# Kernel tuning notes

Measured on AMD Instinct MI355X. Metric: run time of the kernel, lower is better.

Reference implementation:

```python
import jax, jax.numpy as jnp
import numpy as np

B, S, D, H = 2, 2048, 1024, 16
HD = D // H


def setup_inputs() -> dict:
    key = jax.random.key(0)
    ks = jax.random.split(key, 7)
    scale = 1.0 / np.sqrt(D)
    x = jax.random.normal(ks[0], (B, S, D), dtype=jnp.float32)
    att_mask = jax.random.randint(ks[1], (B, S, S), 0, 2, dtype=jnp.int32)
    Wq = jax.random.normal(ks[2], (D, D), dtype=jnp.float32) * scale
    Wk = jax.random.normal(ks[3], (D, D), dtype=jnp.float32) * scale
    Wv = jax.random.normal(ks[4], (D, D), dtype=jnp.float32) * scale
    Wo = jax.random.normal(ks[5], (D, D), dtype=jnp.float32) * scale
    bo = jnp.zeros((D,), dtype=jnp.float32)
    return {"x": x, "att_mask": att_mask, "Wq": Wq, "Wk": Wk, "Wv": Wv, "Wo": Wo, "bo": bo}


def reference(x, att_mask, Wq, Wk, Wv, Wo, bo):
    # Self-attention: kv_source = x, kv_len = q_len = S
    b, s, d = x.shape
    # projections; weights stored as (d_in, d_out)
    q = (x @ Wq).reshape(b, s, H, HD).transpose(0, 2, 1, 3)  # (B,H,S,HD)
    k = (x @ Wk).reshape(b, s, H, HD).transpose(0, 2, 1, 3)
    v = (x @ Wv).reshape(b, s, H, HD).transpose(0, 2, 1, 3)

    scores = jnp.einsum("bhqd,bhkd->bhqk", q, k) / jnp.sqrt(jnp.float32(HD))
    mask = att_mask.astype(bool)[:, None, :, :]  # (B,1,S,S)
    scores = jnp.where(mask, scores, -jnp.inf)

    # Recover fully-masked rows: set their first column score to 0.0
    all_masked = jnp.all(jnp.isneginf(scores), axis=-1, keepdims=True)  # (B,H,S,1)
    first_col = jnp.arange(s) == 0  # (S,)
    scores = jnp.where(all_masked & first_col, 0.0, scores)

    weights = jax.nn.softmax(scores, axis=-1)  # dropout is identity in eval mode
    ctx = jnp.einsum("bhqk,bhkd->bhqd", weights, v)  # (B,H,S,HD)
    ctx = ctx.transpose(0, 2, 1, 3).reshape(b, s, d)
    return ctx @ Wo + bo
```

## Files before the change

### kernel.cpp

```cpp
#include <hip/hip_runtime.h>
#include <stdint.h>

typedef unsigned short u16;
typedef unsigned int u32;
typedef __attribute__((ext_vector_type(8))) short bf16x8;
typedef __attribute__((ext_vector_type(4))) float f32x4;
typedef __attribute__((ext_vector_type(2))) float f32x2;
typedef __attribute__((ext_vector_type(4))) u32 u32x4;

#define MFMA16(a, b, c) __builtin_amdgcn_mfma_f32_16x16x32_bf16((a), (b), (c), 0, 0, 0)

#define QSCALE 0.18033688011112042f

__device__ __forceinline__ u16 f2bf(float f) {
  u32 u = __float_as_uint(f);
  u += 0x7fffu + ((u >> 16) & 1u);
  return (u16)(u >> 16);
}

__device__ __forceinline__ u32 cvt_pk_bf16(float a, float b) {
  u32 r;
  asm("v_cvt_pk_bf16_f32 %0, %1, %2" : "=v"(r) : "v"(a), "v"(b));
  return r;
}

__device__ __forceinline__ void load_lds16(const void* g, void* l) {
  __builtin_amdgcn_global_load_lds((const __attribute__((address_space(1))) void*)g,
                                   (__attribute__((address_space(3))) void*)l, 16, 0, 0);
}

__device__ __forceinline__ int swz8(int row, int cb) {
  return row * 128 + ((cb ^ (row & 7)) << 4);
}

__global__ __launch_bounds__(256) void prep_kernel(const float4* __restrict__ x,
                                                   const int* __restrict__ mask,
                                                   const float* __restrict__ W0,
                                                   const float* __restrict__ W1,
                                                   const float* __restrict__ W2,
                                                   const float* __restrict__ W3,
                                                   ushort4* __restrict__ xbf,
                                                   u16* __restrict__ wt,
                                                   u32* __restrict__ MB) {
  const int bid = blockIdx.x, tid = threadIdx.x;
  __shared__ float t[32][33];
  __shared__ u32 nib[4][64];
  if (bid < 1024) {
    for (int i = bid * 256 + tid; i < 1048576; i += 262144) {
      float4 v = x[i];
      ushort4 o;
      o.x = f2bf(v.x); o.y = f2bf(v.y); o.z = f2bf(v.z); o.w = f2bf(v.w);
      xbf[i] = o;
    }
  } else if (bid < 5120) {
    int r = bid - 1024;
    const int z = r >> 10; r &= 1023;
    const int by = (r >> 5) << 5, bx = (r & 31) << 5;
    const float* W = (z == 0) ? W0 : (z == 1) ? W1 : (z == 2) ? W2 : W3;
    u16* o = wt + (size_t)z * 1048576;
    const int tx = tid & 31, ty = tid >> 5;
#pragma unroll
    for (int j = 0; j < 32; j += 8) t[ty + j][tx] = W[(size_t)(by + ty + j) * 1024 + bx + tx];
    __syncthreads();
#pragma unroll
    for (int j = 0; j < 32; j += 8) o[(size_t)(bx + ty + j) * 1024 + by + tx] = f2bf(t[tx][ty + j]);
  } else {
    const int wave = tid >> 6, lane = tid & 63;
    const int gw = (bid - 5120) * 4 + wave;
    for (int r = gw; r < 32768; r += 4096) {
      const int row = r >> 3, kb = (r & 7) << 8;
      int4 v = *(const int4*)(mask + (size_t)row * 2048 + kb + lane * 4);
      nib[wave][lane] = (v.x ? 1u : 0u) | (v.y ? 2u : 0u) | (v.z ? 4u : 0u) | (v.w ? 8u : 0u);
      if (lane < 8) {
        const u32* p = &nib[wave][lane << 3];
        u32 a = p[0] | (p[1] << 4) | (p[2] << 8) | (p[3] << 12) |
                (p[4] << 16) | (p[5] << 20) | (p[6] << 24) | (p[7] << 28);
        MB[(size_t)row * 64 + (kb >> 5) + lane] = a;
      }
    }
  }
}

template <int MODE>
__global__ __launch_bounds__(256) void gemm_kernel(const u16* __restrict__ A,
                                                   const u16* __restrict__ Bt,
                                                   u16* __restrict__ Qo, u16* __restrict__ Ko,
                                                   u16* __restrict__ Vo, float* __restrict__ Fo,
                                                   const float* __restrict__ bias) {
  __shared__ u16 As[64 * 64];
  __shared__ u16 Bs[128 * 64];
  const int tid = threadIdx.x, lane = tid & 63;
  const int l15 = lane & 15, g = lane >> 4;
  const int wave = tid >> 6, wr = wave >> 1, wc = wave & 1;
  const int bid = blockIdx.x;
  const int xcd = bid & 7, bi = bid >> 3;
  int m0, n0;
  if (MODE == 0) {
    m0 = (((xcd & 3) << 4) + (bi & 15)) * 64;
    n0 = ((xcd >> 2) * 12 + (bi >> 4)) * 128;
  } else {
    m0 = ((xcd << 3) + (bi & 7)) * 64;
    n0 = (bi >> 3) * 128;
  }
  const int xo = (((tid & 7) ^ ((tid >> 3) & 7)) << 4);
  const char* Ag = (const char*)A + (size_t)(m0 + (tid >> 3)) * 2048 + xo;
  const char* Bg = (const char*)Bt + (size_t)(n0 + (tid >> 3)) * 2048 + xo;
  char* Asc = (char*)As;
  char* Bsc = (char*)Bs;
  char* ldA = Asc + wave * 1024;
  char* ldB = Bsc + wave * 1024;

  f32x4 acc[2][4] = {};

  for (int kt = 0; kt < 16; ++kt) {
    const int kbyte = kt * 128;
    __syncthreads();
    load_lds16(Ag + kbyte, ldA);
    load_lds16(Ag + kbyte + 32 * 2048, ldA + 4096);
#pragma unroll
    for (int p = 0; p < 4; ++p)
      load_lds16(Bg + kbyte + p * 65536, ldB + p * 4096);
    __syncthreads();

    bf16x8 af[2][2], bfr[4][2];
#pragma unroll
    for (int i = 0; i < 2; ++i) {
      const int ra = wr * 32 + i * 16 + l15;
      af[i][0] = *(const bf16x8*)(Asc + swz8(ra, g));
      af[i][1] = *(const bf16x8*)(Asc + swz8(ra, 4 + g));
    }
#pragma unroll
    for (int j = 0; j < 4; ++j) {
      const int rb = wc * 64 + j * 16 + l15;
      bfr[j][0] = *(const bf16x8*)(Bsc + swz8(rb, g));
      bfr[j][1] = *(const bf16x8*)(Bsc + swz8(rb, 4 + g));
    }
#pragma unroll
    for (int kk = 0; kk < 2; ++kk)
#pragma unroll
      for (int i = 0; i < 2; ++i)
#pragma unroll
        for (int j = 0; j < 4; ++j)
          acc[i][j] = MFMA16(af[i][kk], bfr[j][kk], acc[i][j]);
  }

  if (MODE == 1) {
#pragma unroll
    for (int i = 0; i < 2; ++i) {
      const int mrow = m0 + wr * 32 + i * 16 + g * 4;
#pragma unroll
      for (int j = 0; j < 4; ++j) {
        const int col = n0 + wc * 64 + j * 16 + l15;
        f32x4 v = acc[i][j];
#pragma unroll
        for (int r = 0; r < 4; ++r)
          Fo[(size_t)(mrow + r) * 1024 + col] = v[r] + bias[col];
      }
    }
  } else {
    const int which = n0 >> 10;
    const float scale = (which == 0) ? QSCALE : 1.0f;
    u16* outp = (which == 0) ? Qo : (which == 1) ? Ko : Vo;
#pragma unroll
    for (int i = 0; i < 2; ++i) {
      const int mrow = m0 + wr * 32 + i * 16 + g * 4;
      const int bb = mrow >> 11, s = mrow & 2047;
#pragma unroll
      for (int j = 0; j < 4; ++j) {
        const int col = (n0 + wc * 64 + j * 16 + l15) & 1023;
        const int h = col >> 6, hd = col & 63;
        f32x4 v = acc[i][j];
        if (which == 2) {
          const int qb = (s >> 2) & 15;
          const int half = (qb >> 2) & 1;
          const int chunk = (qb & 3) | ((qb & 8) >> 1);
          const int sp = (s & ~63) | (chunk << 3) | (half << 2);
          u32 w0 = cvt_pk_bf16(v[0], v[1]);
          u32 w1 = cvt_pk_bf16(v[2], v[3]);
          *(uint2*)(outp + ((((size_t)(bb * 16 + h)) * 64 + hd) * 2048 + sp)) = make_uint2(w0, w1);
        } else {
#pragma unroll
          for (int r = 0; r < 4; ++r)
            outp[(((size_t)(bb * 16 + h)) * 2048 + s + r) * 64 + hd] = f2bf(v[r] * scale);
        }
      }
    }
  }
}

__global__ __launch_bounds__(256, 2) void attn_kernel(const u16* __restrict__ Q,
                                                      const u16* __restrict__ K,
                                                      const u16* __restrict__ VT,
                                                      const u32* __restrict__ MB,
                                                      u16* __restrict__ CTX) {
  __shared__ u16 Kl[2][8192];
  __shared__ u16 Vl[2][8192];
  __shared__ __align__(16) float Mlut[16][4];
  const int tid = threadIdx.x, lane = tid & 63, wave = tid >> 6;
  const int l15 = lane & 15, g = lane >> 4;
  const int L = blockIdx.x + (blockIdx.y << 4);
  const int bh = ((L & 7) << 2) + ((L >> 3) & 3);
  const int q0 = (L >> 5) * 128;
  const int b = bh >> 4, h = bh & 15;
  const int qw0 = q0 + wave * 32;

  const char* Qb = (const char*)Q + ((size_t)bh * 2048 + qw0) * 128;
  const bf16x8 aq00 = *(const bf16x8*)(Qb + l15 * 128 + g * 16);
  const bf16x8 aq01 = *(const bf16x8*)(Qb + l15 * 128 + 64 + g * 16);
  const bf16x8 aq10 = *(const bf16x8*)(Qb + (16 + l15) * 128 + g * 16);
  const bf16x8 aq11 = *(const bf16x8*)(Qb + (16 + l15) * 128 + 64 + g * 16);

  const char* Kg = (const char*)K + (size_t)bh * 2048 * 128;
  const char* Vg = (const char*)VT + (size_t)bh * 64 * 4096;
  const u32* mp0 = MB + ((size_t)b * 2048 + qw0 + l15) * 64;
  const u32* mp1 = mp0 + 16 * 64;

  const int lane8 = lane >> 3;
  const int xo = ((lane & 7) ^ lane8) << 4;
  const char* KsrcL = Kg + (size_t)lane8 * 128 + xo;
  const char* VsrcL = Vg + (size_t)lane8 * 4096 + xo;
  const int vhd = (wave & 1) * 32;
  const int vsub = wave >> 1;

  int koff[4][2], voff[2][4];
#pragma unroll
  for (int i = 0; i < 4; ++i) {
    koff[i][0] = swz8(i * 16 + l15, g);
    koff[i][1] = swz8(i * 16 + l15, 4 + g);
  }
#pragma unroll
  for (int ks = 0; ks < 2; ++ks)
#pragma unroll
    for (int j = 0; j < 4; ++j) voff[ks][j] = swz8(j * 16 + l15, ks * 4 + g);
  const int g4 = g * 4;

  f32x4 oacc[4][2] = {};
  float lrow[2] = {0.f, 0.f};

  if (tid < 16) {
    f32x4 e;
#pragma unroll
    for (int r = 0; r < 4; ++r) e[r] = ((tid >> r) & 1) ? 0.f : -3e38f;
    *(f32x4*)(&Mlut[tid][0]) = e;
  }

  {
    char* Kd = (char*)Kl[0] + wave * 4096;
    char* Vd = (char*)Vl[0] + wave * 4096;
#pragma unroll
    for (int p = 0; p < 4; ++p) {
      load_lds16(KsrcL + wave * 4096 + p * 1024, Kd + p * 1024);
      load_lds16(VsrcL + (size_t)(vhd + p * 8) * 4096 + vsub * 128, Vd + p * 1024);
    }
  }
  uint4 mcA = *(const uint4*)mp0;
  uint4 mcB = *(const uint4*)mp1;
  __syncthreads();

  int cur = 0;
  for (int kb = 0; kb < 16; ++kb) {
    const int kn = (kb < 15) ? kb + 1 : 15;
    if (kb < 15) {
      char* Kd = (cur ? (char*)Kl[0] : (char*)Kl[1]) + wave * 4096;
      char* Vd = (cur ? (char*)Vl[0] : (char*)Vl[1]) + wave * 4096;
#pragma unroll
      for (int p = 0; p < 4; ++p) {
        load_lds16(KsrcL + (size_t)kn * 16384 + wave * 4096 + p * 1024, Kd + p * 1024);
        load_lds16(VsrcL + (size_t)(vhd + p * 8) * 4096 + (size_t)(2 * kn + vsub) * 128,
                   Vd + p * 1024);
      }
    }
    uint4 mnA = *(const uint4*)(mp0 + (size_t)kn * 4);
    uint4 mnB = *(const uint4*)(mp1 + (size_t)kn * 4);

#pragma unroll
    for (int s = 0; s < 2; ++s) {
      const char* Kc = (const char*)Kl[cur] + s * 8192;
      const char* Vc = (const char*)Vl[cur] + s * 8192;
      const u32 mA0 = s ? mcA.z : mcA.x, mA1 = s ? mcA.w : mcA.y;
      const u32 mB0 = s ? mcB.z : mcB.x, mB1 = s ? mcB.w : mcB.y;

      f32x4 sa[2][4];
      __builtin_amdgcn_s_setprio(1);
#pragma unroll
      for (int i = 0; i < 4; ++i) {
        const int sh = (i & 1) * 16 + g4;
        const int nA = (((i & 2) ? mA1 : mA0) >> sh) & 15;
        const int nB = (((i & 2) ? mB1 : mB0) >> sh) & 15;
        f32x4 bA = *(const f32x4*)(&Mlut[nA][0]);
        f32x4 bB = *(const f32x4*)(&Mlut[nB][0]);
        bf16x8 bk0 = *(const bf16x8*)(Kc + koff[i][0]);
        bf16x8 bk1 = *(const bf16x8*)(Kc + koff[i][1]);
        sa[0][i] = MFMA16(bk1, aq01, MFMA16(bk0, aq00, bA));
        sa[1][i] = MFMA16(bk1, aq11, MFMA16(bk0, aq10, bB));
      }
      __builtin_amdgcn_s_setprio(0);

      u32 Wp[2][8];
#pragma unroll
      for (int f = 0; f < 2; ++f) {
        f32x2 ps2 = {0.f, 0.f};
#pragma unroll
        for (int i = 0; i < 4; ++i) {
          const float p0 = __builtin_amdgcn_exp2f(sa[f][i][0]);
          const float p1 = __builtin_amdgcn_exp2f(sa[f][i][1]);
          const float p2 = __builtin_amdgcn_exp2f(sa[f][i][2]);
          const float p3 = __builtin_amdgcn_exp2f(sa[f][i][3]);
          f32x2 a = {p0, p1}, c = {p2, p3};
          ps2 += a + c;
          Wp[f][i * 2] = cvt_pk_bf16(p0, p1);
          Wp[f][i * 2 + 1] = cvt_pk_bf16(p2, p3);
        }
        lrow[f] += ps2.x + ps2.y;
      }

      __builtin_amdgcn_s_setprio(1);
#pragma unroll
      for (int ks = 0; ks < 2; ++ks) {
        u32x4 t0 = {Wp[0][ks * 4], Wp[0][ks * 4 + 1], Wp[0][ks * 4 + 2], Wp[0][ks * 4 + 3]};
        u32x4 t1 = {Wp[1][ks * 4], Wp[1][ks * 4 + 1], Wp[1][ks * 4 + 2], Wp[1][ks * 4 + 3]};
        const bf16x8 ap0 = __builtin_bit_cast(bf16x8, t0);
        const bf16x8 ap1 = __builtin_bit_cast(bf16x8, t1);
#pragma unroll
        for (int j = 0; j < 4; ++j) {
          bf16x8 bv = *(const bf16x8*)(Vc + voff[ks][j]);
          oacc[j][0] = MFMA16(bv, ap0, oacc[j][0]);
          oacc[j][1] = MFMA16(bv, ap1, oacc[j][1]);
        }
      }
      __builtin_amdgcn_s_setprio(0);
      __builtin_amdgcn_sched_barrier(0);
    }

    __syncthreads();
    cur ^= 1;
    mcA = mnA;
    mcB = mnB;
  }

#pragma unroll
  for (int f = 0; f < 2; ++f) {
    float lr = lrow[f];
    lr += __shfl_xor(lr, 16);
    lr += __shfl_xor(lr, 32);
    const float inv = 1.0f / fmaxf(lr, 1e-30f);
    u16* Cb = CTX + ((size_t)(b * 2048 + qw0 + f * 16 + l15)) * 1024 + h * 64 + g * 4;
#pragma unroll
    for (int j = 0; j < 4; ++j) {
      u32 w0 = cvt_pk_bf16(oacc[j][f][0] * inv, oacc[j][f][1] * inv);
      u32 w1 = cvt_pk_bf16(oacc[j][f][2] * inv, oacc[j][f][3] * inv);
      *(uint2*)(Cb + j * 16) = make_uint2(w0, w1);
    }
  }
}

extern "C" void kernel_launch(void* const* d_in, const int* in_sizes, int n_in,
                              void* d_out, int out_size, void* d_ws, size_t ws_size,
                              hipStream_t stream) {
  const float* x   = (const float*)d_in[0];
  const int* amask = (const int*)d_in[1];
  const float* Wq  = (const float*)d_in[2];
  const float* Wk  = (const float*)d_in[3];
  const float* Wv  = (const float*)d_in[4];
  const float* Wo  = (const float*)d_in[5];
  const float* bo  = (const float*)d_in[6];

  char* ws = (char*)d_ws;
  u16* xbf  = (u16*)(ws);
  u16* wt   = (u16*)(ws + 8388608);
  u16* Qb   = (u16*)(ws + 16777216);
  u16* Kb   = (u16*)(ws + 25165824);
  u16* VT   = (u16*)(ws + 33554432);
  u16* CTX  = (u16*)(ws + 41943040);
  u32* MB   = (u32*)(ws + 50331648);

  prep_kernel<<<6144, 256, 0, stream>>>((const float4*)x, amask, Wq, Wk, Wv, Wo,
                                        (ushort4*)xbf, wt, MB);

  gemm_kernel<0><<<1536, 256, 0, stream>>>(xbf, wt, Qb, Kb, VT, nullptr, nullptr);

  attn_kernel<<<dim3(16, 32), 256, 0, stream>>>(Qb, Kb, VT, MB, CTX);

  gemm_kernel<1><<<512, 256, 0, stream>>>(CTX, wt + 3145728, nullptr, nullptr, nullptr,
                                          (float*)d_out, bo);
}
```

Baseline: 116.8 us.

## Single-buffer K/V LDS tiles and raise occupancy to four blocks per CU

Drops the double-buffered K/V LDS staging and keeps a single 32KB buffer, loading the next tile only after the current one is consumed and a barrier is passed. Launch bounds go from 2 to 4 blocks per multiprocessor, so more waves are resident to hide latency. The cost is that global-to-LDS loads no longer overlap with compute inside a block. Each iteration also gains an extra barrier, and the tighter register budget per wave may cause spills.

Measured after the change: 118.3 us. Within noise of the previous version (+1.3%).

```diff
diff --git a/kernel.cpp b/kernel.cpp
--- a/kernel.cpp
+++ b/kernel.cpp
@@ -188,13 +188,13 @@
   }
 }
 
-__global__ __launch_bounds__(256, 2) void attn_kernel(const u16* __restrict__ Q,
+__global__ __launch_bounds__(256, 4) void attn_kernel(const u16* __restrict__ Q,
                                                       const u16* __restrict__ K,
                                                       const u16* __restrict__ VT,
                                                       const u32* __restrict__ MB,
                                                       u16* __restrict__ CTX) {
-  __shared__ u16 Kl[2][8192];
-  __shared__ u16 Vl[2][8192];
+  __shared__ u16 Kl[8192];
+  __shared__ u16 Vl[8192];
   __shared__ __align__(16) float Mlut[16][4];
   const int tid = threadIdx.x, lane = tid & 63, wave = tid >> 6;
   const int l15 = lane & 15, g = lane >> 4;
@@ -244,39 +244,34 @@
     *(f32x4*)(&Mlut[tid][0]) = e;
   }
 
-  {
-    char* Kd = (char*)Kl[0] + wave * 4096;
-    char* Vd = (char*)Vl[0] + wave * 4096;
-#pragma unroll
-    for (int p = 0; p < 4; ++p) {
-      load_lds16(KsrcL + wave * 4096 + p * 1024, Kd + p * 1024);
-      load_lds16(VsrcL + (size_t)(vhd + p * 8) * 4096 + vsub * 128, Vd + p * 1024);
-    }
-  }
+#define STAGE(kbv)                                                                    \
+  {                                                                                   \
+    char* Kd = (char*)Kl + wave * 4096;                                               \
+    char* Vd = (char*)Vl + wave * 4096;                                               \
+    _Pragma("unroll")                                                                 \
+    for (int p = 0; p < 4; ++p) {                                                     \
+      load_lds16(KsrcL + (size_t)(kbv) * 16384 + wave * 4096 + p * 1024,              \
+                 Kd + p * 1024);                                                      \
+      load_lds16(VsrcL + (size_t)(vhd + p * 8) * 4096 + (size_t)(2 * (kbv) + vsub) * 128, \
+                 Vd + p * 1024);                                                      \
+    }                                                                                 \
+  }
+
+  STAGE(0)
   uint4 mcA = *(const uint4*)mp0;
   uint4 mcB = *(const uint4*)mp1;
-  __syncthreads();
-
-  int cur = 0;
+
   for (int kb = 0; kb < 16; ++kb) {
+    __syncthreads();
+
     const int kn = (kb < 15) ? kb + 1 : 15;
-    if (kb < 15) {
-      char* Kd = (cur ? (char*)Kl[0] : (char*)Kl[1]) + wave * 4096;
-      char* Vd = (cur ? (char*)Vl[0] : (char*)Vl[1]) + wave * 4096;
-#pragma unroll
-      for (int p = 0; p < 4; ++p) {
-        load_lds16(KsrcL + (size_t)kn * 16384 + wave * 4096 + p * 1024, Kd + p * 1024);
-        load_lds16(VsrcL + (size_t)(vhd + p * 8) * 4096 + (size_t)(2 * kn + vsub) * 128,
-                   Vd + p * 1024);
-      }
-    }
     uint4 mnA = *(const uint4*)(mp0 + (size_t)kn * 4);
     uint4 mnB = *(const uint4*)(mp1 + (size_t)kn * 4);
 
 #pragma unroll
     for (int s = 0; s < 2; ++s) {
-      const char* Kc = (const char*)Kl[cur] + s * 8192;
-      const char* Vc = (const char*)Vl[cur] + s * 8192;
+      const char* Kc = (const char*)Kl + s * 8192;
+      const char* Vc = (const char*)Vl + s * 8192;
       const u32 mA0 = s ? mcA.z : mcA.x, mA1 = s ? mcA.w : mcA.y;
       const u32 mB0 = s ? mcB.z : mcB.x, mB1 = s ? mcB.w : mcB.y;
 
@@ -333,10 +328,11 @@
     }
 
     __syncthreads();
-    cur ^= 1;
+    if (kb < 15) STAGE(kb + 1)
     mcA = mnA;
     mcB = mnB;
   }
+#undef STAGE
 
 #pragma unroll
   for (int f = 0; f < 2; ++f) {
```
